# Optimization experiments

Hardware: AMD Instinct MI355X
Metric: run time of the kernel (lower is better)

## Reference

```python
import jax, jax.numpy as jnp
import numpy as np

N_QUBITS = 10
N_LAYERS = 2
QSVT_DEGREE = 3
DT_RANK = 5  # n_qubits // 2
PI = np.float32(np.pi)

# ---- batched statevector simulation helpers (wire 0 = most significant, as in pennylane default.qubit) ----

def _apply_1q(s, wire, U):
    # s: (batch,) + (2,)*n complex; U: (batch,2,2) or (2,2)
    s = jnp.moveaxis(s, 1 + wire, 1)
    shp = s.shape
    s2 = s.reshape(shp[0], 2, -1)
    if U.ndim == 3:
        out = jnp.einsum('bij,bjr->bir', U, s2)
    else:
        out = jnp.einsum('ij,bjr->bir', U, s2)
    return jnp.moveaxis(out.reshape(shp), 1, 1 + wire)

def _ry(t):
    c = jnp.cos(t / 2).astype(jnp.complex64)
    s = jnp.sin(t / 2).astype(jnp.complex64)
    return jnp.stack([jnp.stack([c, -s], -1), jnp.stack([s, c], -1)], -2)

def _rz(t):
    e = jnp.exp(-0.5j * jnp.asarray(t).astype(jnp.complex64))
    z = jnp.zeros_like(e)
    return jnp.stack([jnp.stack([e, z], -1), jnp.stack([z, jnp.conj(e)], -1)], -2)

def _rx(t):
    c = jnp.cos(t / 2).astype(jnp.complex64)
    s = (-1j) * jnp.sin(t / 2).astype(jnp.complex64)
    return jnp.stack([jnp.stack([c, s], -1), jnp.stack([s, c], -1)], -2)

def _cnot(s, control, target):
    f = jnp.flip(s, axis=1 + target)
    s0 = jax.lax.index_in_dim(s, 0, axis=1 + control, keepdims=True)
    f1 = jax.lax.index_in_dim(f, 1, axis=1 + control, keepdims=True)
    return jnp.concatenate([s0, f1], axis=1 + control)

def _circuit(h, x, dt, cp, pc):
    """Batched selective QSVT circuit; h,x,dt: (B,n). Returns <Z_i> per wire, (B,n) float32."""
    n = N_QUBITS
    b = h.shape[0]
    s = jnp.zeros((b, 2 ** n), jnp.complex64).at[:, 0].set(1.0).reshape((b,) + (2,) * n)
    # 1. state encoding
    for i in range(n):
        s = _apply_1q(s, i, _ry(h[:, i]))
    # 2. delta-modulated QSVT block
    for d in range(QSVT_DEGREE + 1):
        for i in range(n):
            s = _apply_1q(s, i, _rz(pc[d] * dt[:, i] * PI))
        for i in range(n - 1):
            s = _cnot(s, i, i + 1)
        s = _cnot(s, n - 1, 0)
    # 3. variational block
    k = 0
    for _ in range(N_LAYERS):
        for i in range(n):
            s = _apply_1q(s, i, _rx(cp[k]))
            s = _apply_1q(s, i, _ry(cp[k + 1]))
            s = _apply_1q(s, i, _rz(cp[k + 2]))
            k += 3
        for i in range(n - 1):
            s = _cnot(s, i, i + 1)
    # 4. delta-modulated input encoding
    for i in range(n):
        s = _apply_1q(s, i, _ry(x[:, i] * dt[:, i]))
    # 5. <Z_i> measurements
    p = s.real ** 2 + s.imag ** 2
    zs = [(jax.lax.index_in_dim(p, 0, 1 + i, False) - jax.lax.index_in_dim(p, 1, 1 + i, False)).reshape(b, -1).sum(-1) for i in range(n)]
    return jnp.stack(zs, -1).astype(jnp.float32)

def setup_inputs() -> dict:
    key = jax.random.key(0)
    ks = jax.random.split(key, 6)
    B, S, n, r = 128, 512, N_QUBITS, DT_RANK
    angles = jax.random.uniform(ks[0], (B, S, n), jnp.float32) * PI  # angle encoding in [0, pi]
    W_x = jax.random.normal(ks[1], (r + 2 * n, n), jnp.float32) * 0.3  # x_proj weight (no bias)
    W_dt = jax.random.normal(ks[2], (n, r), jnp.float32) * 0.3  # dt_proj weight
    rng = np.random.default_rng(0)
    dt0 = np.exp(rng.random(n) * (np.log(0.1) - np.log(0.001)) + np.log(0.001))
    b_dt = jnp.asarray(dt0 + np.log(-np.expm1(-dt0)), jnp.float32)  # inverse-softplus init
    poly_coeffs = jax.random.normal(ks[3], (QSVT_DEGREE + 1,), jnp.float32) * 0.1
    circuit_params = jax.random.normal(ks[4], (n * N_LAYERS * 3,), jnp.float32) * 0.1
    D = jnp.ones((n,), jnp.float32)
    return {"angles": angles, "W_x": W_x, "W_dt": W_dt, "b_dt": b_dt,
            "poly_coeffs": poly_coeffs, "circuit_params": circuit_params, "D": D}

def reference(angles, W_x, W_dt, b_dt, poly_coeffs, circuit_params, D):
    # selective projections
    x_dbc = jnp.einsum('bsn,kn->bsk', angles, W_x)
    dt_raw = x_dbc[..., :DT_RANK]
    # B slice (x_dbc[..., DT_RANK:DT_RANK+n]) is computed but unused in the original forward
    C = x_dbc[..., DT_RANK + N_QUBITS:]
    dt = jax.nn.softplus(jnp.einsum('bsr,nr->bsn', dt_raw, W_dt) + b_dt)
    dt_angles = jnp.tanh(dt) * PI
    # quantum recurrence uses detached tensors in the original (torch .detach())
    x_sg = jax.lax.stop_gradient(angles)
    dt_sg = jax.lax.stop_gradient(dt_angles)
    cp = jax.lax.stop_gradient(circuit_params)
    pc = jax.lax.stop_gradient(poly_coeffs)

    def step(h, xs):
        x_t, d_t = xs
        h2 = _circuit(h, x_t, d_t, cp, pc)
        return h2, h2

    h0 = jnp.zeros((angles.shape[0], N_QUBITS), jnp.float32)
    _, hs = jax.lax.scan(step, h0, (jnp.swapaxes(x_sg, 0, 1), jnp.swapaxes(dt_sg, 0, 1)))
    hs = jnp.swapaxes(hs, 0, 1)  # (B,S,n)
    return C * hs + D * angles
```

## Files before the change

kernel.cpp:

```cpp
#include <hip/hip_runtime.h>
#include <math.h>


#define PIF 3.14159265358979323846f

constexpr int NQ = 10, SEQ = 512, NB = 128, NTHR = 512, RECF = 36;

struct CTbl { int mz[4][NQ]; };
constexpr CTbl build_tbl() {
  CTbl t{};
  unsigned mrow[NQ];
  for (int b = 0; b < NQ; ++b) mrow[b] = 1u << b;
  for (int d = 0; d < 4; ++d) {
    for (int i = 0; i < NQ; ++i) t.mz[d][i] = (int)mrow[9 - i];
    for (int i = 0; i < NQ - 1; ++i) { int bc = 9 - i, bt = 8 - i; mrow[bt] ^= mrow[bc]; }
    mrow[9] ^= mrow[0];
  }
  return t;
}
constexpr CTbl CT = build_tbl();

struct PermCols { int c4[10]; int cL[10]; };
constexpr PermCols build_perms() {
  PermCols P{};
  for (int b = 0; b < 10; ++b) {
    int x = 1 << b;
    for (int d = 0; d < 4; ++d) {
      for (int i = 0; i < 9; ++i) { int bc = 9 - i, bt = 8 - i; if ((x >> bc) & 1) x ^= (1 << bt); }
      if (x & 1) x ^= (1 << 9);
    }
    P.c4[b] = x;
    int y = 1 << b;
    for (int i = 0; i < 9; ++i) { int bc = 9 - i, bt = 8 - i; if ((y >> bc) & 1) y ^= (1 << bt); }
    P.cL[b] = y;
  }
  return P;
}
constexpr PermCols PC = build_perms();

constexpr int lanePart(int x)  { return ((x >> 0) & 1) | (((x >> 5) & 1) << 1) |
                                        (((x >> 1) & 1) << 2) | (((x >> 7) & 1) << 3) |
                                        (((x >> 3) & 1) << 4) | (((x >> 9) & 1) << 5); }
constexpr int wavePart8(int x) { return ((x >> 4) & 1) | (((x >> 8) & 1) << 1) |
                                        (((x >> 6) & 1) << 2); }

typedef __attribute__((ext_vector_type(2))) float v2;

constexpr int VOFS[8] = {0, 16, 256, 272, 64, 80, 320, 336};

template<int C>
__device__ __forceinline__ int dpp1(int x) {
  return __builtin_amdgcn_update_dpp(x, x, C, 0xF, 0xF, false);
}
template<int VL>
__device__ __forceinline__ int lxi(int x) {
  if constexpr (VL == 1)  return dpp1<0xB1>(x);
  else if constexpr (VL == 2)  return dpp1<0x4E>(x);
  else if constexpr (VL == 3)  return dpp1<0x1B>(x);
  else if constexpr (VL <= 7) {
    constexpr int q = (VL & 3) ^ 3;
    int y = x;
    if constexpr (q == 1) y = dpp1<0xB1>(y);
    else if constexpr (q == 2) y = dpp1<0x4E>(y);
    else if constexpr (q == 3) y = dpp1<0x1B>(y);
    return dpp1<0x141>(y);
  } else if constexpr (VL >= 12) {
    constexpr int q = (VL & 3) ^ 3;
    int y = x;
    if constexpr (q == 1) y = dpp1<0xB1>(y);
    else if constexpr (q == 2) y = dpp1<0x4E>(y);
    else if constexpr (q == 3) y = dpp1<0x1B>(y);
    return dpp1<0x140>(y);
  } else {
    constexpr int a = VL & 3;
    int y = x;
    if constexpr (a == 1) y = dpp1<0xB1>(y);
    else if constexpr (a == 2) y = dpp1<0x4E>(y);
    else if constexpr (a == 3) y = dpp1<0x1B>(y);
    y = dpp1<0x141>(y);
    return dpp1<0x140>(y);
  }
}
template<int VL>
__device__ __forceinline__ float lx(float x) {
  if constexpr (VL == 0) return x;
  else if constexpr (VL & 32) {
    int addr = (((int)threadIdx.x & 63) ^ VL) << 2;
    return __int_as_float(__builtin_amdgcn_ds_bpermute(addr, __float_as_int(x)));
  } else if constexpr (VL & 16) {
    return __int_as_float(__builtin_amdgcn_ds_swizzle(__float_as_int(x), (VL << 10) | 0x1F));
  } else {
    return __int_as_float(lxi<VL>(__float_as_int(x)));
  }
}
__device__ __forceinline__ float rdl(float x, int l) {
  return __int_as_float(__builtin_amdgcn_readlane(__float_as_int(x), l));
}

__device__ __forceinline__ int swz(int j) {
  return j ^ (((j >> 5) & 1) << 2) ^ ((j >> 7) & 1);
}

__device__ __forceinline__ void apply2(v2* amp, const v2* p, bool par, float4 U0, float4 U1) {
  v2 u00 = {U0.x, U0.y}, u01 = {U0.z, U0.w}, u10 = {U1.x, U1.y}, u11 = {U1.z, U1.w};
  v2 A = par ? u11 : u00, B = par ? u10 : u01;
  v2 An = {-A.y, A.y}, Bn = {-B.y, B.y};
#pragma unroll
  for (int r = 0; r < 2; ++r) {
    v2 o = amp[r], q = p[r];
    v2 res = A.x * o;
    res += An * __builtin_shufflevector(o, o, 1, 0);
    res += B.x * q;
    res += Bn * __builtin_shufflevector(q, q, 1, 0);
    amp[r] = res;
  }
}

template<int VL>
__device__ __forceinline__ void gate_lane2(v2* amp, float4 U0, float4 U1, int lane) {
  v2 p[2];
#pragma unroll
  for (int r = 0; r < 2; ++r) { p[r].x = lx<VL>(amp[r].x); p[r].y = lx<VL>(amp[r].y); }
  apply2(amp, p, (lane & VL) != 0, U0, U1);
}

__device__ __forceinline__ void gate_reg1(v2* amp, float4 U0, float4 U1) {
  v2 u00 = {U0.x, U0.y}, u01 = {U0.z, U0.w}, u10 = {U1.x, U1.y}, u11 = {U1.z, U1.w};
  v2 o0 = amp[0], o1 = amp[1];
  v2 a0 = {0.f, 0.f}, a1 = {0.f, 0.f};
  a0.x += u00.x * o0.x - u00.y * o0.y;  a0.y += u00.x * o0.y + u00.y * o0.x;
  a0.x += u01.x * o1.x - u01.y * o1.y;  a0.y += u01.x * o1.y + u01.y * o1.x;
  a1.x += u10.x * o0.x - u10.y * o0.y;  a1.y += u10.x * o0.y + u10.y * o0.x;
  a1.x += u11.x * o1.x - u11.y * o1.y;  a1.y += u11.x * o1.y + u11.y * o1.x;
  amp[0] = a0; amp[1] = a1;
}

template<int VL>
__device__ __forceinline__ float xdot_lane2(const v2* amp) {
  v2 acc = {0.f, 0.f};
#pragma unroll
  for (int r = 0; r < 2; ++r) {
    v2 p; p.x = lx<VL>(amp[r].x); p.y = lx<VL>(amp[r].y);
    acc += amp[r] * p;
  }
  return acc.x + acc.y;
}

__global__ __launch_bounds__(NTHR, 2) void qmamba_main(
    const float* __restrict__ angles, const float* __restrict__ Wx,
    const float* __restrict__ Wdt, const float* __restrict__ bdt,
    const float* __restrict__ pc, const float* __restrict__ cp,
    float* __restrict__ out)
{
  __shared__ float  tblL[SEQ][RECF];
  __shared__ float4 uuL[40];
  __shared__ v2     ex0[1024];
  __shared__ v2     ex1[1024];
  __shared__ float  zb[8][16];

  const int tid  = threadIdx.x;
  const int lane = tid & 63;
  const int wave = tid >> 6;
  const int b    = blockIdx.x;

  if (tid < 20) {
    int k = tid * 3;
    float al = 0.5f * cp[k], be = 0.5f * cp[k + 1], ga = 0.5f * cp[k + 2];
    float ca = __cosf(al), sa = __sinf(al);
    float cb = __cosf(be), sb = __sinf(be);
    float cg = __cosf(ga), sg = __sinf(ga);
    float2 M00 = make_float2(cb * ca,  sb * sa);
    float2 M01 = make_float2(-sb * ca, -cb * sa);
    float2 M10 = make_float2(sb * ca,  -cb * sa);
    float2 M11 = make_float2(cb * ca,  -sb * sa);
    float2 e0 = make_float2(cg, -sg), e1 = make_float2(cg, sg);
    auto cm = [](float2 a, float2 c) {
      return make_float2(a.x * c.x - a.y * c.y, a.x * c.y + a.y * c.x);
    };
    float2 u00 = cm(M00, e0), u01 = cm(M01, e0), u10 = cm(M10, e1), u11 = cm(M11, e1);
    uuL[2 * tid]     = make_float4(u00.x, u00.y, u01.x, u01.y);
    uuL[2 * tid + 1] = make_float4(u10.x, u10.y, u11.x, u11.y);
  }

  {
    const int t = tid;
    const float* ar = angles + (size_t)(b * SEQ + t) * NQ;
    float a[NQ];
#pragma unroll
    for (int n = 0; n < NQ; ++n) a[n] = ar[n];
    float dtr[5];
#pragma unroll
    for (int r = 0; r < 5; ++r) {
      float acc = 0.f;
#pragma unroll
      for (int n = 0; n < NQ; ++n) acc += a[n] * Wx[r * NQ + n];
      dtr[r] = acc;
    }
    float* rec = &tblL[t][0];
#pragma unroll
    for (int w = 0; w < NQ; ++w) {
      float lin = bdt[w];
#pragma unroll
      for (int r = 0; r < 5; ++r) lin += dtr[r] * Wdt[w * 5 + r];
      float sp = lin > 0.f ? lin + log1pf(__expf(-lin)) : log1pf(__expf(lin));
      float th = tanhf(sp) * PIF;
      float fa = a[w] * th;
      rec[w]      = th;
      rec[12 + w] = __cosf(fa);
      rec[24 + w] = __sinf(fa);
    }
  }
  __syncthreads();

  float pch[4];
#pragma unroll
  for (int d = 0; d < 4; ++d) pch[d] = 0.5f * pc[d] * PIF;

  v2 cw0[8], cw1[8];
  {
    const int s5 = wave & 1, s1 = (wave >> 1) & 1, s3 = (wave >> 2) & 1;
    auto ent = [&](int g, int row, int col) -> v2 {
      float4 R = uuL[2 * g + row];
      return col ? v2{R.z, R.w} : v2{R.x, R.y};
    };
    auto cmul = [](v2 a, v2 c) -> v2 {
      return v2{a.x * c.x - a.y * c.y, a.x * c.y + a.y * c.x};
    };
#pragma unroll
    for (int v = 0; v < 8; ++v) {
      const int v5 = v & 1, v1 = (v >> 1) & 1, v3 = (v >> 2) & 1;
      cw0[v] = cmul(cmul(ent(5,  s5, s5 ^ v5), ent(1,  s1, s1 ^ v1)), ent(3,  s3, s3 ^ v3));
      cw1[v] = cmul(cmul(ent(15, s5, s5 ^ v5), ent(11, s1, s1 ^ v1)), ent(13, s3, s3 ^ v3));
    }
  }

  unsigned PW0 = 0, PW1 = 0;
#pragma unroll
  for (int k = 0; k < 40; ++k) {
    const int m  = CT.mz[k / 10][k % 10];
    const int lm = lanePart(m), wm = wavePart8(m);
    unsigned flip = ((unsigned)((__popc(lane & lm) ^ __popc(wave & wm)) & 1)) ^ 1u;
    if (k < 32) PW0 |= flip << k; else PW1 |= flip << (k - 32);
  }

  int d4 = 0, dL = 0;
  if (lane & 1)  { d4 ^= PC.c4[0]; dL ^= PC.cL[0]; }
  if (lane & 2)  { d4 ^= PC.c4[5]; dL ^= PC.cL[5]; }
  if (lane & 4)  { d4 ^= PC.c4[1]; dL ^= PC.cL[1]; }
  if (lane & 8)  { d4 ^= PC.c4[7]; dL ^= PC.cL[7]; }
  if (lane & 16) { d4 ^= PC.c4[3]; dL ^= PC.cL[3]; }
  if (lane & 32) { d4 ^= PC.c4[9]; dL ^= PC.cL[9]; }
  if (wave & 1)  { d4 ^= PC.c4[4]; dL ^= PC.cL[4]; }
  if (wave & 2)  { d4 ^= PC.c4[8]; dL ^= PC.cL[8]; }
  if (wave & 4)  { d4 ^= PC.c4[6]; dL ^= PC.cL[6]; }
  const int oR4 = PC.c4[2], oRL = PC.cL[2];

  const int oidx = (lane & 1) | (((lane >> 1) & 1) << 5) | (((lane >> 2) & 1) << 1)
                 | (((lane >> 3) & 1) << 7) | (((lane >> 4) & 1) << 3) | (((lane >> 5) & 1) << 9)
                 | ((wave & 1) << 4) | (((wave >> 1) & 1) << 8) | (((wave >> 2) & 1) << 6);

  float hcw[NQ], hsw[NQ];
#pragma unroll
  for (int w = 0; w < NQ; ++w) { hcw[w] = 1.f; hsw[w] = 0.f; }

  v2 amp[2];

#pragma unroll 1
  for (int t = 0; t < SEQ; ++t) {
    float tha[12];
    {
      const float4* rq = (const float4*)&tblL[t][0];
#pragma unroll
      for (int j = 0; j < 3; ++j) ((float4*)tha)[j] = rq[j];
    }

    float F;
    F  = (lane & 1)  ? hsw[9] : hcw[9];
    F *= (lane & 2)  ? hsw[4] : hcw[4];
    F *= (lane & 4)  ? hsw[8] : hcw[8];
    F *= (lane & 8)  ? hsw[2] : hcw[2];
    F *= (lane & 16) ? hsw[6] : hcw[6];
    F *= (lane & 32) ? hsw[0] : hcw[0];
    F *= (wave & 1)  ? hsw[5] : hcw[5];
    F *= (wave & 2)  ? hsw[1] : hcw[1];
    F *= (wave & 4)  ? hsw[3] : hcw[3];
    const float G0 = F * hcw[7];
    const float G1 = F * hsw[7];

    float S0 = 0.f, S1 = 0.f;
#pragma unroll
    for (int k = 0; k < 40; ++k) {
      const int m  = CT.mz[k / 10][k % 10];
      float v = pch[k / 10] * tha[k % 10];
      unsigned fl = ((k < 32 ? (PW0 >> k) : (PW1 >> (k - 32))) & 1u) << 31;
      float sv = __int_as_float(__float_as_int(v) ^ fl);
      if ((m >> 2) & 1) S1 += sv; else S0 += sv;
    }
    {
      float sn, cs;
      __sincosf(S0 + S1, &sn, &cs); amp[0].x = G0 * cs; amp[0].y = G0 * sn;
      __sincosf(S0 - S1, &sn, &cs); amp[1].x = G1 * cs; amp[1].y = G1 * sn;
    }

    ex0[swz(d4)]       = amp[0];
    ex0[swz(d4 ^ oR4)] = amp[1];
    __syncthreads();
    {
      v2 pv0[8], pv1[8];
#pragma unroll
      for (int v = 0; v < 8; ++v) {
        const int base = oidx ^ VOFS[v];
        pv0[v] = ex0[swz(base)];
        pv1[v] = ex0[swz(base | 4)];
      }
      v2 a0 = {0.f, 0.f}, a1 = {0.f, 0.f};
#pragma unroll
      for (int v = 0; v < 8; ++v) {
        v2 c = cw0[v];
        a0.x += c.x * pv0[v].x - c.y * pv0[v].y;
        a0.y += c.x * pv0[v].y + c.y * pv0[v].x;
        a1.x += c.x * pv1[v].x - c.y * pv1[v].y;
        a1.y += c.x * pv1[v].y + c.y * pv1[v].x;
      }
      amp[0] = a0; amp[1] = a1;
    }
    gate_lane2<32>(amp, uuL[0],  uuL[1],  lane);
    gate_lane2<8> (amp, uuL[4],  uuL[5],  lane);
    gate_lane2<2> (amp, uuL[8],  uuL[9],  lane);
    gate_lane2<16>(amp, uuL[12], uuL[13], lane);
    gate_reg1     (amp, uuL[14], uuL[15]);
    gate_lane2<4> (amp, uuL[16], uuL[17], lane);
    gate_lane2<1> (amp, uuL[18], uuL[19], lane);

    ex1[swz(dL)]       = amp[0];
    ex1[swz(dL ^ oRL)] = amp[1];
    __syncthreads();
    {
      v2 pv0[8], pv1[8];
#pragma unroll
      for (int v = 0; v < 8; ++v) {
        const int base = oidx ^ VOFS[v];
        pv0[v] = ex1[swz(base)];
        pv1[v] = ex1[swz(base | 4)];
      }
      v2 a0 = {0.f, 0.f}, a1 = {0.f, 0.f};
#pragma unroll
      for (int v = 0; v < 8; ++v) {
        v2 c = cw1[v];
        a0.x += c.x * pv0[v].x - c.y * pv0[v].y;
        a0.y += c.x * pv0[v].y + c.y * pv0[v].x;
        a1.x += c.x * pv1[v].x - c.y * pv1[v].y;
        a1.y += c.x * pv1[v].y + c.y * pv1[v].x;
      }
      amp[0] = a0; amp[1] = a1;
    }
    gate_lane2<32>(amp, uuL[20], uuL[21], lane);
    gate_lane2<8> (amp, uuL[24], uuL[25], lane);
    gate_lane2<2> (amp, uuL[28], uuL[29], lane);
    gate_lane2<16>(amp, uuL[32], uuL[33], lane);
    gate_reg1     (amp, uuL[34], uuL[35]);
    gate_lane2<4> (amp, uuL[36], uuL[37], lane);
    gate_lane2<1> (amp, uuL[38], uuL[39], lane);

    ex0[swz(dL)]       = amp[0];
    ex0[swz(dL ^ oRL)] = amp[1];
    __syncthreads();
    v2 pw5[2], pw1[2], pw3[2];
    amp[0] = ex0[swz(oidx)];
    amp[1] = ex0[swz(oidx | 4)];
    pw5[0] = ex0[swz(oidx ^ 16)];   pw5[1] = ex0[swz((oidx ^ 16) | 4)];
    pw1[0] = ex0[swz(oidx ^ 256)];  pw1[1] = ex0[swz((oidx ^ 256) | 4)];
    pw3[0] = ex0[swz(oidx ^ 64)];   pw3[1] = ex0[swz((oidx ^ 64) | 4)];

    float cfv[12], sfv[12];
    {
      const float4* rq = (const float4*)&tblL[t][0];
#pragma unroll
      for (int j = 0; j < 3; ++j) { ((float4*)cfv)[j] = rq[3 + j]; ((float4*)sfv)[j] = rq[6 + j]; }
    }

    const float n0 = amp[0].x * amp[0].x + amp[0].y * amp[0].y;
    const float n1 = amp[1].x * amp[1].x + amp[1].y * amp[1].y;
    const float T0 = n0 + n1;
    const float T1 = n0 - n1;

    auto vdot2 = [](const v2* a, const v2* p) {
      v2 acc = a[0] * p[0] + a[1] * p[1];
      return acc.x + acc.y;
    };

    float zv[NQ];
    { float zp = (lane & 32) ? -T0 : T0; zv[0] = cfv[0] * zp - sfv[0] * xdot_lane2<32>(amp); }
    { float zp = (wave & 2)  ? -T0 : T0; zv[1] = cfv[1] * zp - sfv[1] * vdot2(amp, pw1); }
    { float zp = (lane & 8)  ? -T0 : T0; zv[2] = cfv[2] * zp - sfv[2] * xdot_lane2<8>(amp); }
    { float zp = (wave & 4)  ? -T0 : T0; zv[3] = cfv[3] * zp - sfv[3] * vdot2(amp, pw3); }
    { float zp = (lane & 2)  ? -T0 : T0; zv[4] = cfv[4] * zp - sfv[4] * xdot_lane2<2>(amp); }
    { float zp = (wave & 1)  ? -T0 : T0; zv[5] = cfv[5] * zp - sfv[5] * vdot2(amp, pw5); }
    { float zp = (lane & 16) ? -T0 : T0; zv[6] = cfv[6] * zp - sfv[6] * xdot_lane2<16>(amp); }
    { float xr = 2.f * (amp[0].x * amp[1].x + amp[0].y * amp[1].y);
      zv[7] = cfv[7] * T1 - sfv[7] * xr; }
    { float zp = (lane & 4)  ? -T0 : T0; zv[8] = cfv[8] * zp - sfv[8] * xdot_lane2<4>(amp); }
    { float zp = (lane & 1)  ? -T0 : T0; zv[9] = cfv[9] * zp - sfv[9] * xdot_lane2<1>(amp); }

#pragma unroll
    for (int w = 0; w < NQ; ++w) {
      zv[w] += lx<1>(zv[w]);
      zv[w] += lx<2>(zv[w]);
      zv[w] += lx<4>(zv[w]);
    }
    const int l7 = lane & 7;
    float c01 = (l7 & 1) ? zv[1] : zv[0];
    float c23 = (l7 & 1) ? zv[3] : zv[2];
    float c45 = (l7 & 1) ? zv[5] : zv[4];
    float c67 = (l7 & 1) ? zv[7] : zv[6];
    float c03 = (l7 & 2) ? c23 : c01;
    float c47 = (l7 & 2) ? c67 : c45;
    float pk  = (l7 & 4) ? c47 : c03;
    pk += lx<8>(pk);  pk += lx<16>(pk);  pk += lx<32>(pk);
    float z8 = zv[8]; z8 += lx<8>(z8); z8 += lx<16>(z8); z8 += lx<32>(z8);
    float z9 = zv[9]; z9 += lx<8>(z9); z9 += lx<16>(z9); z9 += lx<32>(z9);
    float zsel = pk;
    zsel = (lane == 8) ? z8 : zsel;
    zsel = (lane == 9) ? z9 : zsel;

    if (lane < NQ) zb[wave][lane] = zsel;
    __syncthreads();
    float z = 0.f;
    if (lane < NQ) {
      z = zb[0][lane] + zb[1][lane] + zb[2][lane] + zb[3][lane]
        + zb[4][lane] + zb[5][lane] + zb[6][lane] + zb[7][lane];
      if (wave == 0) out[(size_t)(b * SEQ + t) * NQ + lane] = z;
    }
    float sn_h, cs_h;
    __sincosf(0.5f * z, &sn_h, &cs_h);
#pragma unroll
    for (int w = 0; w < NQ; ++w) { hcw[w] = rdl(cs_h, w); hsw[w] = rdl(sn_h, w); }
  }
}

__global__ __launch_bounds__(256) void qmamba_post(
    const float* __restrict__ angles, const float* __restrict__ Wx,
    const float* __restrict__ Dg, float* __restrict__ out)
{
  int i = blockIdx.x * 256 + threadIdx.x;
  if (i >= NB * SEQ * NQ) return;
  int w  = i % NQ;
  int bt = i / NQ;
  const float* a = angles + (size_t)bt * NQ;
  float C = 0.f;
#pragma unroll
  for (int n = 0; n < NQ; ++n) C += a[n] * Wx[(15 + w) * NQ + n];
  float z = out[i];
  out[i] = C * z + Dg[w] * a[w];
}

extern "C" void kernel_launch(void* const* d_in, const int* in_sizes, int n_in,
                              void* d_out, int out_size, void* d_ws, size_t ws_size,
                              hipStream_t stream) {
  (void)in_sizes; (void)n_in; (void)out_size; (void)d_ws; (void)ws_size;
  const float* angles = (const float*)d_in[0];
  const float* Wx     = (const float*)d_in[1];
  const float* Wdt    = (const float*)d_in[2];
  const float* bdt    = (const float*)d_in[3];
  const float* pc     = (const float*)d_in[4];
  const float* cp     = (const float*)d_in[5];
  const float* Dg     = (const float*)d_in[6];
  float* out = (float*)d_out;
  hipLaunchKernelGGL(qmamba_main, dim3(NB), dim3(NTHR), 0, stream,
                     angles, Wx, Wdt, bdt, pc, cp, out);
  hipLaunchKernelGGL(qmamba_post, dim3((NB * SEQ * NQ + 255) / 256), dim3(256), 0, stream,
                     angles, Wx, Dg, out);
}
```

Baseline: 2.221 ms.

## Remap LDS exchange layout for float4 loads and precompute per-lane gate coefficients

Changes the shared-memory exchange buffers to a new index mapping (kmap plus swzk swizzle) so each thread's two amplitudes sit together and can be read with single float4 loads instead of many scalar v2 loads. It also hoists the per-lane gate coefficient selection out of the sequential loop into registers, folds the 40-term phase sum into precomputed per-qubit weights, and replaces sign selects with XOR masks. Launch bounds drop to one block per SIMD occupancy hint, which frees more registers for the hoisted constants at the cost of occupancy hints.

```diff
diff --git a/kernel.cpp b/kernel.cpp
--- a/kernel.cpp
+++ b/kernel.cpp
@@ -44,9 +44,18 @@
 constexpr int wavePart8(int x) { return ((x >> 4) & 1) | (((x >> 8) & 1) << 1) |
                                         (((x >> 6) & 1) << 2); }
 
+constexpr int kmap(int x) {
+  return ((x >> 2) & 1)
+       | (((x >> 0) & 1) << 1) | (((x >> 5) & 1) << 2) | (((x >> 1) & 1) << 3)
+       | (((x >> 7) & 1) << 4) | (((x >> 3) & 1) << 5) | (((x >> 9) & 1) << 6)
+       | (((x >> 4) & 1) << 7) | (((x >> 8) & 1) << 8) | (((x >> 6) & 1) << 9);
+}
+constexpr int swzk(int k) { return k ^ (((k >> 5) & 1) << 1) ^ (((k >> 4) & 1) << 2); }
+
+constexpr int SKC4 = swzk(kmap(PC.c4[2]));
+constexpr int SKCL = swzk(kmap(PC.cL[2]));
+
 typedef __attribute__((ext_vector_type(2))) float v2;
-
-constexpr int VOFS[8] = {0, 16, 256, 272, 64, 80, 320, 336};
 
 template<int C>
 __device__ __forceinline__ int dpp1(int x) {
@@ -97,41 +106,28 @@
   return __int_as_float(__builtin_amdgcn_readlane(__float_as_int(x), l));
 }
 
-__device__ __forceinline__ int swz(int j) {
-  return j ^ (((j >> 5) & 1) << 2) ^ ((j >> 7) & 1);
-}
-
-__device__ __forceinline__ void apply2(v2* amp, const v2* p, bool par, float4 U0, float4 U1) {
-  v2 u00 = {U0.x, U0.y}, u01 = {U0.z, U0.w}, u10 = {U1.x, U1.y}, u11 = {U1.z, U1.w};
-  v2 A = par ? u11 : u00, B = par ? u10 : u01;
-  v2 An = {-A.y, A.y}, Bn = {-B.y, B.y};
-#pragma unroll
-  for (int r = 0; r < 2; ++r) {
-    v2 o = amp[r], q = p[r];
-    v2 res = A.x * o;
-    res += An * __builtin_shufflevector(o, o, 1, 0);
-    res += B.x * q;
-    res += Bn * __builtin_shufflevector(q, q, 1, 0);
-    amp[r] = res;
-  }
-}
+struct GC { float Ax, Ay, Bx, By; };
 
 template<int VL>
-__device__ __forceinline__ void gate_lane2(v2* amp, float4 U0, float4 U1, int lane) {
-  v2 p[2];
-#pragma unroll
-  for (int r = 0; r < 2; ++r) { p[r].x = lx<VL>(amp[r].x); p[r].y = lx<VL>(amp[r].y); }
-  apply2(amp, p, (lane & VL) != 0, U0, U1);
+__device__ __forceinline__ void gateh(v2* amp, const GC& g) {
+  v2 p0, p1;
+  p0.x = lx<VL>(amp[0].x); p0.y = lx<VL>(amp[0].y);
+  p1.x = lx<VL>(amp[1].x); p1.y = lx<VL>(amp[1].y);
+  v2 o0 = amp[0], o1 = amp[1];
+  amp[0].x = g.Ax * o0.x - g.Ay * o0.y + g.Bx * p0.x - g.By * p0.y;
+  amp[0].y = g.Ax * o0.y + g.Ay * o0.x + g.Bx * p0.y + g.By * p0.x;
+  amp[1].x = g.Ax * o1.x - g.Ay * o1.y + g.Bx * p1.x - g.By * p1.y;
+  amp[1].y = g.Ax * o1.y + g.Ay * o1.x + g.Bx * p1.y + g.By * p1.x;
 }
 
 __device__ __forceinline__ void gate_reg1(v2* amp, float4 U0, float4 U1) {
   v2 u00 = {U0.x, U0.y}, u01 = {U0.z, U0.w}, u10 = {U1.x, U1.y}, u11 = {U1.z, U1.w};
   v2 o0 = amp[0], o1 = amp[1];
-  v2 a0 = {0.f, 0.f}, a1 = {0.f, 0.f};
-  a0.x += u00.x * o0.x - u00.y * o0.y;  a0.y += u00.x * o0.y + u00.y * o0.x;
-  a0.x += u01.x * o1.x - u01.y * o1.y;  a0.y += u01.x * o1.y + u01.y * o1.x;
-  a1.x += u10.x * o0.x - u10.y * o0.y;  a1.y += u10.x * o0.y + u10.y * o0.x;
-  a1.x += u11.x * o1.x - u11.y * o1.y;  a1.y += u11.x * o1.y + u11.y * o1.x;
+  v2 a0, a1;
+  a0.x = u00.x * o0.x - u00.y * o0.y + u01.x * o1.x - u01.y * o1.y;
+  a0.y = u00.x * o0.y + u00.y * o0.x + u01.x * o1.y + u01.y * o1.x;
+  a1.x = u10.x * o0.x - u10.y * o0.y + u11.x * o1.x - u11.y * o1.y;
+  a1.y = u10.x * o0.y + u10.y * o0.x + u11.x * o1.y + u11.y * o1.x;
   amp[0] = a0; amp[1] = a1;
 }
 
@@ -146,7 +142,7 @@
   return acc.x + acc.y;
 }
 
-__global__ __launch_bounds__(NTHR, 2) void qmamba_main(
+__global__ __launch_bounds__(NTHR, 1) void qmamba_main(
     const float* __restrict__ angles, const float* __restrict__ Wx,
     const float* __restrict__ Wdt, const float* __restrict__ bdt,
     const float* __restrict__ pc, const float* __restrict__ cp,
@@ -154,8 +150,8 @@
 {
   __shared__ float  tblL[SEQ][RECF];
   __shared__ float4 uuL[40];
-  __shared__ v2     ex0[1024];
-  __shared__ v2     ex1[1024];
+  __shared__ __align__(16) v2 ex0[1024];
+  __shared__ __align__(16) v2 ex1[1024];
   __shared__ float  zb[8][16];
 
   const int tid  = threadIdx.x;
@@ -212,9 +208,6 @@
   }
   __syncthreads();
 
-  float pch[4];
-#pragma unroll
-  for (int d = 0; d < 4; ++d) pch[d] = 0.5f * pc[d] * PIF;
 
   v2 cw0[8], cw1[8];
   {
@@ -234,30 +227,66 @@
     }
   }
 
-  unsigned PW0 = 0, PW1 = 0;
-#pragma unroll
-  for (int k = 0; k < 40; ++k) {
-    const int m  = CT.mz[k / 10][k % 10];
-    const int lm = lanePart(m), wm = wavePart8(m);
-    unsigned flip = ((unsigned)((__popc(lane & lm) ^ __popc(wave & wm)) & 1)) ^ 1u;
-    if (k < 32) PW0 |= flip << k; else PW1 |= flip << (k - 32);
-  }
-
-  int d4 = 0, dL = 0;
-  if (lane & 1)  { d4 ^= PC.c4[0]; dL ^= PC.cL[0]; }
-  if (lane & 2)  { d4 ^= PC.c4[5]; dL ^= PC.cL[5]; }
-  if (lane & 4)  { d4 ^= PC.c4[1]; dL ^= PC.cL[1]; }
-  if (lane & 8)  { d4 ^= PC.c4[7]; dL ^= PC.cL[7]; }
-  if (lane & 16) { d4 ^= PC.c4[3]; dL ^= PC.cL[3]; }
-  if (lane & 32) { d4 ^= PC.c4[9]; dL ^= PC.cL[9]; }
-  if (wave & 1)  { d4 ^= PC.c4[4]; dL ^= PC.cL[4]; }
-  if (wave & 2)  { d4 ^= PC.c4[8]; dL ^= PC.cL[8]; }
-  if (wave & 4)  { d4 ^= PC.c4[6]; dL ^= PC.cL[6]; }
-  const int oR4 = PC.c4[2], oRL = PC.cL[2];
-
-  const int oidx = (lane & 1) | (((lane >> 1) & 1) << 5) | (((lane >> 2) & 1) << 1)
-                 | (((lane >> 3) & 1) << 7) | (((lane >> 4) & 1) << 3) | (((lane >> 5) & 1) << 9)
-                 | ((wave & 1) << 4) | (((wave >> 1) & 1) << 8) | (((wave >> 2) & 1) << 6);
+  GC gc[12];
+  {
+    auto mk = [&](int VL, int g) -> GC {
+      float4 U0 = uuL[2 * g], U1 = uuL[2 * g + 1];
+      bool par = (lane & VL) != 0;
+      GC r;
+      r.Ax = par ? U1.z : U0.x;  r.Ay = par ? U1.w : U0.y;
+      r.Bx = par ? U1.x : U0.z;  r.By = par ? U1.y : U0.w;
+      return r;
+    };
+    gc[0]  = mk(32, 0);  gc[1]  = mk(8, 2);   gc[2]  = mk(2, 4);
+    gc[3]  = mk(16, 6);  gc[4]  = mk(4, 8);   gc[5]  = mk(1, 9);
+    gc[6]  = mk(32, 10); gc[7]  = mk(8, 12);  gc[8]  = mk(2, 14);
+    gc[9]  = mk(16, 16); gc[10] = mk(4, 18);  gc[11] = mk(1, 19);
+  }
+  const float4 rga0 = uuL[14], rga1 = uuL[15];
+  const float4 rgb0 = uuL[34], rgb1 = uuL[35];
+
+  float pch[4];
+#pragma unroll
+  for (int d = 0; d < 4; ++d) pch[d] = 0.5f * pc[d] * PIF;
+  float Kp[NQ], Km[NQ];
+#pragma unroll
+  for (int i = 0; i < NQ; ++i) {
+    float k0 = 0.f, k1 = 0.f;
+#pragma unroll
+    for (int d = 0; d < 4; ++d) {
+      const int m  = CT.mz[d][i];
+      const int lm = lanePart(m), wm = wavePart8(m);
+      const int rb = (m >> 2) & 1;
+      const int p0 = (__popc(lane & lm) ^ __popc(wave & wm)) & 1;
+      k0 += p0 ? pch[d] : -pch[d];
+      k1 += (p0 ^ rb) ? pch[d] : -pch[d];
+    }
+    Kp[i] = k0; Km[i] = k1;
+  }
+
+  int d4k = 0, dLk = 0;
+  if (lane & 1)  { d4k ^= kmap(PC.c4[0]); dLk ^= kmap(PC.cL[0]); }
+  if (lane & 2)  { d4k ^= kmap(PC.c4[5]); dLk ^= kmap(PC.cL[5]); }
+  if (lane & 4)  { d4k ^= kmap(PC.c4[1]); dLk ^= kmap(PC.cL[1]); }
+  if (lane & 8)  { d4k ^= kmap(PC.c4[7]); dLk ^= kmap(PC.cL[7]); }
+  if (lane & 16) { d4k ^= kmap(PC.c4[3]); dLk ^= kmap(PC.cL[3]); }
+  if (lane & 32) { d4k ^= kmap(PC.c4[9]); dLk ^= kmap(PC.cL[9]); }
+  if (wave & 1)  { d4k ^= kmap(PC.c4[4]); dLk ^= kmap(PC.cL[4]); }
+  if (wave & 2)  { d4k ^= kmap(PC.c4[8]); dLk ^= kmap(PC.cL[8]); }
+  if (wave & 4)  { d4k ^= kmap(PC.c4[6]); dLk ^= kmap(PC.cL[6]); }
+  const int sd4  = swzk(d4k);
+  const int sdL  = swzk(dLk);
+  const int sown = swzk((lane << 1) | (wave << 7));
+
+  const unsigned sm0 = (lane & 32) ? 0x80000000u : 0u;
+  const unsigned sm1 = (wave & 2)  ? 0x80000000u : 0u;
+  const unsigned sm2 = (lane & 8)  ? 0x80000000u : 0u;
+  const unsigned sm3 = (wave & 4)  ? 0x80000000u : 0u;
+  const unsigned sm4 = (lane & 2)  ? 0x80000000u : 0u;
+  const unsigned sm5 = (wave & 1)  ? 0x80000000u : 0u;
+  const unsigned sm6 = (lane & 16) ? 0x80000000u : 0u;
+  const unsigned sm8 = (lane & 4)  ? 0x80000000u : 0u;
+  const unsigned sm9 = (lane & 1)  ? 0x80000000u : 0u;
 
   float hcw[NQ], hsw[NQ];
 #pragma unroll
@@ -287,90 +316,76 @@
     const float G0 = F * hcw[7];
     const float G1 = F * hsw[7];
 
-    float S0 = 0.f, S1 = 0.f;
-#pragma unroll
-    for (int k = 0; k < 40; ++k) {
-      const int m  = CT.mz[k / 10][k % 10];
-      float v = pch[k / 10] * tha[k % 10];
-      unsigned fl = ((k < 32 ? (PW0 >> k) : (PW1 >> (k - 32))) & 1u) << 31;
-      float sv = __int_as_float(__float_as_int(v) ^ fl);
-      if ((m >> 2) & 1) S1 += sv; else S0 += sv;
-    }
+    float Sa = 0.f, Sb = 0.f;
+#pragma unroll
+    for (int i = 0; i < NQ; ++i) { Sa += Kp[i] * tha[i]; Sb += Km[i] * tha[i]; }
     {
       float sn, cs;
-      __sincosf(S0 + S1, &sn, &cs); amp[0].x = G0 * cs; amp[0].y = G0 * sn;
-      __sincosf(S0 - S1, &sn, &cs); amp[1].x = G1 * cs; amp[1].y = G1 * sn;
-    }
-
-    ex0[swz(d4)]       = amp[0];
-    ex0[swz(d4 ^ oR4)] = amp[1];
+      __sincosf(Sa, &sn, &cs); amp[0].x = G0 * cs; amp[0].y = G0 * sn;
+      __sincosf(Sb, &sn, &cs); amp[1].x = G1 * cs; amp[1].y = G1 * sn;
+    }
+
+    ex0[sd4]        = amp[0];
+    ex0[sd4 ^ SKC4] = amp[1];
     __syncthreads();
     {
-      v2 pv0[8], pv1[8];
+      const float4* q4 = (const float4*)ex0;
+      v2 a0 = {0.f, 0.f}, a1 = {0.f, 0.f};
 #pragma unroll
       for (int v = 0; v < 8; ++v) {
-        const int base = oidx ^ VOFS[v];
-        pv0[v] = ex0[swz(base)];
-        pv1[v] = ex0[swz(base | 4)];
-      }
-      v2 a0 = {0.f, 0.f}, a1 = {0.f, 0.f};
-#pragma unroll
-      for (int v = 0; v < 8; ++v) {
+        float4 q = q4[(sown ^ (v << 7)) >> 1];
         v2 c = cw0[v];
-        a0.x += c.x * pv0[v].x - c.y * pv0[v].y;
-        a0.y += c.x * pv0[v].y + c.y * pv0[v].x;
-        a1.x += c.x * pv1[v].x - c.y * pv1[v].y;
-        a1.y += c.x * pv1[v].y + c.y * pv1[v].x;
+        a0.x += c.x * q.x - c.y * q.y;  a0.y += c.x * q.y + c.y * q.x;
+        a1.x += c.x * q.z - c.y * q.w;  a1.y += c.x * q.w + c.y * q.z;
       }
       amp[0] = a0; amp[1] = a1;
     }
-    gate_lane2<32>(amp, uuL[0],  uuL[1],  lane);
-    gate_lane2<8> (amp, uuL[4],  uuL[5],  lane);
-    gate_lane2<2> (amp, uuL[8],  uuL[9],  lane);
-    gate_lane2<16>(amp, uuL[12], uuL[13], lane);
-    gate_reg1     (amp, uuL[14], uuL[15]);
-    gate_lane2<4> (amp, uuL[16], uuL[17], lane);
-    gate_lane2<1> (amp, uuL[18], uuL[19], lane);
-
-    ex1[swz(dL)]       = amp[0];
-    ex1[swz(dL ^ oRL)] = amp[1];
+    gateh<32>(amp, gc[0]);
+    gateh<8> (amp, gc[1]);
+    gateh<2> (amp, gc[2]);
+    gateh<16>(amp, gc[3]);
+    gate_reg1(amp, rga0, rga1);
+    gateh<4> (amp, gc[4]);
+    gateh<1> (amp, gc[5]);
+
+    ex1[sdL]        = amp[0];
+    ex1[sdL ^ SKCL] = amp[1];
     __syncthreads();
     {
-      v2 pv0[8], pv1[8];
+      const float4* q4 = (const float4*)ex1;
+      v2 a0 = {0.f, 0.f}, a1 = {0.f, 0.f};
 #pragma unroll
       for (int v = 0; v < 8; ++v) {
-        const int base = oidx ^ VOFS[v];
-        pv0[v] = ex1[swz(base)];
-        pv1[v] = ex1[swz(base | 4)];
-      }
-      v2 a0 = {0.f, 0.f}, a1 = {0.f, 0.f};
-#pragma unroll
-      for (int v = 0; v < 8; ++v) {
+        float4 q = q4[(sown ^ (v << 7)) >> 1];
         v2 c = cw1[v];
-        a0.x += c.x * pv0[v].x - c.y * pv0[v].y;
-        a0.y += c.x * pv0[v].y + c.y * pv0[v].x;
-        a1.x += c.x * pv1[v].x - c.y * pv1[v].y;
-        a1.y += c.x * pv1[v].y + c.y * pv1[v].x;
+        a0.x += c.x * q.x - c.y * q.y;  a0.y += c.x * q.y + c.y * q.x;
+        a1.x += c.x * q.z - c.y * q.w;  a1.y += c.x * q.w + c.y * q.z;
       }
       amp[0] = a0; amp[1] = a1;
     }
-    gate_lane2<32>(amp, uuL[20], uuL[21], lane);
-    gate_lane2<8> (amp, uuL[24], uuL[25], lane);
-    gate_lane2<2> (amp, uuL[28], uuL[29], lane);
-    gate_lane2<16>(amp, uuL[32], uuL[33], lane);
-    gate_reg1     (amp, uuL[34], uuL[35]);
-    gate_lane2<4> (amp, uuL[36], uuL[37], lane);
-    gate_lane2<1> (amp, uuL[38], uuL[39], lane);
-
-    ex0[swz(dL)]       = amp[0];
-    ex0[swz(dL ^ oRL)] = amp[1];
+    gateh<32>(amp, gc[6]);
+    gateh<8> (amp, gc[7]);
+    gateh<2> (amp, gc[8]);
+    gateh<16>(amp, gc[9]);
+    gate_reg1(amp, rgb0, rgb1);
+    gateh<4> (amp, gc[10]);
+    gateh<1> (amp, gc[11]);
+
+    ex0[sdL]        = amp[0];
+    ex0[sdL ^ SKCL] = amp[1];
     __syncthreads();
     v2 pw5[2], pw1[2], pw3[2];
-    amp[0] = ex0[swz(oidx)];
-    amp[1] = ex0[swz(oidx | 4)];
-    pw5[0] = ex0[swz(oidx ^ 16)];   pw5[1] = ex0[swz((oidx ^ 16) | 4)];
-    pw1[0] = ex0[swz(oidx ^ 256)];  pw1[1] = ex0[swz((oidx ^ 256) | 4)];
-    pw3[0] = ex0[swz(oidx ^ 64)];   pw3[1] = ex0[swz((oidx ^ 64) | 4)];
+    {
+      const float4* q4 = (const float4*)ex0;
+      float4 qs = q4[sown >> 1];
+      float4 q5 = q4[(sown ^ (1 << 7)) >> 1];
+      float4 q1 = q4[(sown ^ (2 << 7)) >> 1];
+      float4 q3 = q4[(sown ^ (4 << 7)) >> 1];
+      amp[0] = v2{qs.x, qs.y}; amp[1] = v2{qs.z, qs.w};
+      pw5[0] = v2{q5.x, q5.y}; pw5[1] = v2{q5.z, q5.w};
+      pw1[0] = v2{q1.x, q1.y}; pw1[1] = v2{q1.z, q1.w};
+      pw3[0] = v2{q3.x, q3.y}; pw3[1] = v2{q3.z, q3.w};
+    }
 
     float cfv[12], sfv[12];
     {
@@ -383,6 +398,7 @@
     const float n1 = amp[1].x * amp[1].x + amp[1].y * amp[1].y;
     const float T0 = n0 + n1;
     const float T1 = n0 - n1;
+    const int   T0i = __float_as_int(T0);
 
     auto vdot2 = [](const v2* a, const v2* p) {
       v2 acc = a[0] * p[0] + a[1] * p[1];
@@ -390,17 +406,17 @@
     };
 
     float zv[NQ];
-    { float zp = (lane & 32) ? -T0 : T0; zv[0] = cfv[0] * zp - sfv[0] * xdot_lane2<32>(amp); }
-    { float zp = (wave & 2)  ? -T0 : T0; zv[1] = cfv[1] * zp - sfv[1] * vdot2(amp, pw1); }
-    { float zp = (lane & 8)  ? -T0 : T0; zv[2] = cfv[2] * zp - sfv[2] * xdot_lane2<8>(amp); }
-    { float zp = (wave & 4)  ? -T0 : T0; zv[3] = cfv[3] * zp - sfv[3] * vdot2(amp, pw3); }
-    { float zp = (lane & 2)  ? -T0 : T0; zv[4] = cfv[4] * zp - sfv[4] * xdot_lane2<2>(amp); }
-    { float zp = (wave & 1)  ? -T0 : T0; zv[5] = cfv[5] * zp - sfv[5] * vdot2(amp, pw5); }
-    { float zp = (lane & 16) ? -T0 : T0; zv[6] = cfv[6] * zp - sfv[6] * xdot_lane2<16>(amp); }
+    zv[0] = cfv[0] * __int_as_float(T0i ^ sm0) - sfv[0] * xdot_lane2<32>(amp);
+    zv[1] = cfv[1] * __int_as_float(T0i ^ sm1) - sfv[1] * vdot2(amp, pw1);
+    zv[2] = cfv[2] * __int_as_float(T0i ^ sm2) - sfv[2] * xdot_lane2<8>(amp);
+    zv[3] = cfv[3] * __int_as_float(T0i ^ sm3) - sfv[3] * vdot2(amp, pw3);
+    zv[4] = cfv[4] * __int_as_float(T0i ^ sm4) - sfv[4] * xdot_lane2<2>(amp);
+    zv[5] = cfv[5] * __int_as_float(T0i ^ sm5) - sfv[5] * vdot2(amp, pw5);
+    zv[6] = cfv[6] * __int_as_float(T0i ^ sm6) - sfv[6] * xdot_lane2<16>(amp);
     { float xr = 2.f * (amp[0].x * amp[1].x + amp[0].y * amp[1].y);
       zv[7] = cfv[7] * T1 - sfv[7] * xr; }
-    { float zp = (lane & 4)  ? -T0 : T0; zv[8] = cfv[8] * zp - sfv[8] * xdot_lane2<4>(amp); }
-    { float zp = (lane & 1)  ? -T0 : T0; zv[9] = cfv[9] * zp - sfv[9] * xdot_lane2<1>(amp); }
+    zv[8] = cfv[8] * __int_as_float(T0i ^ sm8) - sfv[8] * xdot_lane2<4>(amp);
+    zv[9] = cfv[9] * __int_as_float(T0i ^ sm9) - sfv[9] * xdot_lane2<1>(amp);
 
 #pragma unroll
     for (int w = 0; w < NQ; ++w) {
```

New measurement: 3.434 ms. 54.6% more time.
